# Optimization experiments

Measured on AMD Instinct MI355X. Metric: run time of the kernel, lower is better.

Reference implementation:

```python
import jax, jax.numpy as jnp
import numpy as np

DIM = 512
HEADS = 8
HEAD_DIM = DIM // HEADS
SCALE = HEAD_DIM ** -0.5
LN_EPS = 1e-5


def _layernorm(t, g, b):
    mu = jnp.mean(t, axis=-1, keepdims=True)
    var = jnp.mean(jnp.square(t - mu), axis=-1, keepdims=True)
    return (t - mu) * jax.lax.rsqrt(var + LN_EPS) * g + b


def setup_inputs() -> dict:
    key = jax.random.key(0)
    ks = jax.random.split(key, 8)
    B, C, H, W = 2, DIM, 48, 48
    s = 1.0 / np.sqrt(DIM)
    return {
        "x": jax.random.normal(ks[0], (B, C, H, W), jnp.float32),
        "y": jax.random.normal(ks[1], (B, C, H, W), jnp.float32),
        # linear weights stored [in, out]
        "k_w": jax.random.uniform(ks[2], (DIM, DIM), jnp.float32, -s, s),
        "k_b": jax.random.uniform(ks[3], (DIM,), jnp.float32, -s, s),
        "qv_w": jax.random.uniform(ks[4], (DIM, 2 * DIM), jnp.float32, -s, s),
        "qv_b": jax.random.uniform(ks[5], (2 * DIM,), jnp.float32, -s, s),
        "lnx_g": jnp.ones((DIM,), jnp.float32),
        "lnx_b": jnp.zeros((DIM,), jnp.float32),
        "lny_g": jnp.ones((DIM,), jnp.float32),
        "lny_b": jnp.zeros((DIM,), jnp.float32),
    }


def _split_qv(t, qv_w, qv_b):
    B, N, C = t.shape
    qv = (t @ qv_w + qv_b).reshape(B, N, 2, HEADS, HEAD_DIM)
    qv = jnp.transpose(qv, (2, 0, 3, 1, 4))  # [2, B, h, N, d]
    return qv[0], qv[1]


def _heads(t):
    B, N, C = t.shape
    return jnp.transpose(t.reshape(B, N, HEADS, HEAD_DIM), (0, 2, 1, 3))  # [B,h,N,d]


def reference(x, y, k_w, k_b, qv_w, qv_b, lnx_g, lnx_b, lny_g, lny_b):
    B, C = x.shape[0], x.shape[1]
    xf = _layernorm(jnp.transpose(x.reshape(B, C, -1), (0, 2, 1)), lnx_g, lnx_b)  # [B,N,C]
    yf = _layernorm(jnp.transpose(y.reshape(B, C, -1), (0, 2, 1)), lny_g, lny_b)
    N = xf.shape[1]

    y_q, y_v = _split_qv(yf, qv_w, qv_b)
    x_q, x_v = _split_qv(xf, qv_w, qv_b)
    y_k = _heads(yf @ k_w + k_b)
    x_k = _heads(xf @ k_w + k_b)

    # branch 1: softmax(x_q y_k^T) x_v  -> standard [B,N,C]
    a1 = jax.nn.softmax(jnp.einsum('bhnd,bhmd->bhnm', x_q, y_k) * SCALE, axis=-1)
    xo = jnp.einsum('bhnm,bhmd->bhnd', a1, x_v)
    xo = jnp.transpose(xo, (0, 2, 1, 3)).reshape(B, N, C)

    # branch 2: faithful reproduction of torch quirk (x_k kept a leading 1-dim,
    # so the output [1,B,h,N,d].transpose(1,2).reshape(B,N,C) scrambles layout)
    a2 = jax.nn.softmax(jnp.einsum('bhnd,bhmd->bhnm', y_q, x_k) * SCALE, axis=-1)
    yo = jnp.einsum('bhnm,bhmd->bhnd', a2, y_v)  # [B,h,N,d]
    yo = jnp.transpose(yo[None], (0, 2, 1, 3, 4)).reshape(B, N, C)

    return jnp.concatenate([xo, yo], axis=0)  # [2B, N, C]
```

## Files before the change

### kernel.cpp

```cpp
#include <hip/hip_runtime.h>

#define DIM 512
#define NTOK 2304
#define HEADS 8
#define HD 64
#define LN_EPS 1e-5f
#define BNC 2359296
#define QSC 0.18033688011112042f

typedef __attribute__((ext_vector_type(8))) short short8;
typedef __attribute__((ext_vector_type(4))) short sh4;
typedef __attribute__((ext_vector_type(4))) float f32x4;

__device__ __forceinline__ short f2bf(float f) {
    union { float f; unsigned u; } x; x.f = f;
    unsigned r = (x.u + 0x7fffu + ((x.u >> 16) & 1u)) >> 16;
    return (short)(r & 0xffffu);
}
__device__ __forceinline__ unsigned fbits(float f) {
    union { float f; unsigned u; } x; x.f = f; return x.u;
}
__device__ __forceinline__ void gl2lds(const short* g, short* l) {
    __builtin_amdgcn_global_load_lds(
        (const __attribute__((address_space(1))) unsigned int*)g,
        (__attribute__((address_space(3))) unsigned int*)l, 16, 0, 0);
}

__global__ void k_prep(const float* __restrict__ x, const float* __restrict__ y,
                       float* __restrict__ mu, float* __restrict__ rs,
                       const float* __restrict__ qv_w, const float* __restrict__ k_w,
                       const float* __restrict__ qv_b, const float* __restrict__ k_b,
                       short* __restrict__ Wt, float* __restrict__ bias) {
    __shared__ __align__(16) float tile[64][65];
    __shared__ float pS[4][64], pQ[4][64];
    int bx = blockIdx.x, tid = threadIdx.x;
    if (bx < 144) {
        int nt = bx % 36, sb = bx / 36;
        int nl = tid & 63, part = tid >> 6;
        int n = nt * 64 + nl;
        int s = sb >> 1, b = sb & 1;
        const float* src = (s ? y : x) + (size_t)b * DIM * NTOK + n;
        float sum = 0.f, sq = 0.f;
        for (int c = part * 128; c < part * 128 + 128; c++) {
            float v = src[(size_t)c * NTOK];
            sum += v; sq += v * v;
        }
        pS[part][nl] = sum; pQ[part][nl] = sq;
        __syncthreads();
        if (tid < 64) {
            float ts = pS[0][tid] + pS[1][tid] + pS[2][tid] + pS[3][tid];
            float tq = pQ[0][tid] + pQ[1][tid] + pQ[2][tid] + pQ[3][tid];
            float m = ts * (1.0f / DIM);
            float var = tq * (1.0f / DIM) - m * m;
            mu[sb * NTOK + nt * 64 + tid] = m;
            rs[sb * NTOK + nt * 64 + tid] = rsqrtf(var + LN_EPS);
        }
        return;
    }
    int idx = bx - 144;
    int jt = idx % 24, ct = idx / 24;
    int j0 = jt * 64, c0 = ct * 64;
    if (ct == 0 && tid < 64) {
        int j = j0 + tid;
        bias[j] = (j < 1024) ? qv_b[j] : k_b[j - 1024];
    }
    for (int slot = tid; slot < 1024; slot += 256) {
        int r = slot >> 4, q = slot & 15;
        int c = c0 + r;
        float4 v;
        if (j0 < 1024) v = *(const float4*)(qv_w + (size_t)c * 1024 + j0 + q * 4);
        else           v = *(const float4*)(k_w  + (size_t)c * 512  + (j0 - 1024) + q * 4);
        tile[r][q*4+0] = v.x; tile[r][q*4+1] = v.y;
        tile[r][q*4+2] = v.z; tile[r][q*4+3] = v.w;
    }
    __syncthreads();
    int jr = tid >> 2, cg = tid & 3;
    short8 o0, o1;
    for (int i = 0; i < 8; i++) o0[i] = f2bf(tile[cg*16+i][jr]);
    for (int i = 0; i < 8; i++) o1[i] = f2bf(tile[cg*16+8+i][jr]);
    short* dst = Wt + (size_t)(j0 + jr) * DIM + c0 + cg * 16;
    *(short8*)dst = o0;
    *(short8*)(dst + 8) = o1;
}

__global__ void k_normT(const float* __restrict__ x, const float* __restrict__ y,
                        const float* __restrict__ mu, const float* __restrict__ rs,
                        const float* __restrict__ gx, const float* __restrict__ bx,
                        const float* __restrict__ gy, const float* __restrict__ by,
                        short* __restrict__ T) {
    __shared__ __align__(16) float tile[64][65];
    int nt = blockIdx.x, ct = blockIdx.y, sb = blockIdx.z;
    int s = sb >> 1, b = sb & 1;
    int n0 = nt * 64, c0 = ct * 64;
    const float* src = (s ? y : x) + (size_t)b * DIM * NTOK;
    int tid = threadIdx.x;
    for (int slot = tid; slot < 1024; slot += 256) {
        int r = slot >> 4, q = slot & 15;
        const float* p = src + (size_t)(c0 + r) * NTOK + n0 + q * 4;
        float4 v = *(const float4*)p;
        tile[r][q*4+0] = v.x; tile[r][q*4+1] = v.y;
        tile[r][q*4+2] = v.z; tile[r][q*4+3] = v.w;
    }
    __syncthreads();
    const float* g  = s ? gy : gx;
    const float* be = s ? by : bx;
    int nr = tid >> 2, cg = tid & 3;
    int n = n0 + nr;
    float m = mu[sb * NTOK + n], r_ = rs[sb * NTOK + n];
    short8 o0, o1;
    for (int i = 0; i < 8; i++) {
        int c = c0 + cg * 16 + i;
        o0[i] = f2bf((tile[cg*16+i][nr] - m) * r_ * g[c] + be[c]);
    }
    for (int i = 0; i < 8; i++) {
        int c = c0 + cg * 16 + 8 + i;
        o1[i] = f2bf((tile[cg*16+8+i][nr] - m) * r_ * g[c] + be[c]);
    }
    short* dst = T + ((size_t)sb * NTOK + n) * DIM + c0 + cg * 16;
    *(short8*)dst = o0;
    *(short8*)(dst + 8) = o1;
}

__global__ void __launch_bounds__(256)
k_gemm(const short* __restrict__ T, const short* __restrict__ Wt,
       const float* __restrict__ bias, short* __restrict__ QVK,
       short* __restrict__ VT) {
    __shared__ __align__(16) short smem[2 * 128 * 64];
    short* As = smem;
    short* Bs = smem + 128 * 64;
    int n0 = blockIdx.x * 128, j0 = blockIdx.y * 128, sb = blockIdx.z;
    int tid = threadIdx.x;
    int w = tid >> 6, l = tid & 63;
    int wr = w >> 1, wc = w & 1;
    int lrow = l & 15, quad = l >> 4;
    int r_in = (l >> 3) & 7, cc = l & 7;
    int ch = cc ^ r_in;
    int sw0 = (quad ^ (lrow & 7)) * 8;
    const short* Ab = T + (size_t)sb * NTOK * DIM;
    f32x4 acc[4][4] = {};
    for (int kk = 0; kk < 8; kk++) {
        if (kk) __syncthreads();
        for (int inst = 0; inst < 4; inst++) {
            int R = w * 32 + inst * 8 + r_in;
            gl2lds(Ab + (size_t)(n0 + R) * 512 + kk * 64 + ch * 8,
                   &As[(w * 32 + inst * 8) * 64]);
            gl2lds(Wt + (size_t)(j0 + R) * 512 + kk * 64 + ch * 8,
                   &Bs[(w * 32 + inst * 8) * 64]);
        }
        __syncthreads();
        for (int c2 = 0; c2 < 2; c2++) {
            int off = c2 ? (sw0 ^ 32) : sw0;
            short8 af[4], bf[4];
            for (int i = 0; i < 4; i++)
                af[i] = *(const short8*)&As[(wr*64 + i*16 + lrow) * 64 + off];
            for (int j = 0; j < 4; j++)
                bf[j] = *(const short8*)&Bs[(wc*64 + j*16 + lrow) * 64 + off];
            for (int i = 0; i < 4; i++)
                for (int j = 0; j < 4; j++)
                    acc[i][j] = __builtin_amdgcn_mfma_f32_16x16x32_bf16(af[i], bf[j], acc[i][j], 0, 0, 0);
        }
    }
    if (j0 >= 512 && j0 < 1024) {
        __syncthreads();
        for (int i = 0; i < 4; i++)
            for (int j = 0; j < 4; j++) {
                int jloc = wc * 64 + j * 16 + lrow;
                float bv = bias[j0 + jloc];
                int nloc = wr * 64 + i * 16 + quad * 4;
                int c8 = nloc >> 3, half = (nloc >> 2) & 1;
                sh4 pk;
                for (int reg = 0; reg < 4; reg++) pk[reg] = f2bf(acc[i][j][reg] + bv);
                *(sh4*)&smem[jloc * 128 + ((c8 ^ (jloc & 15)) * 8) + half * 4] = pk;
            }
        __syncthreads();
        for (int slot = tid; slot < 2048; slot += 256) {
            int row = slot >> 4, seg = slot & 15;
            short8 v = *(const short8*)&smem[row * 128 + ((seg ^ (row & 15)) * 8)];
            *(short8*)(VT + ((size_t)sb * 512 + (j0 - 512) + row) * NTOK + n0 + seg * 8) = v;
        }
    } else {
        for (int i = 0; i < 4; i++)
            for (int j = 0; j < 4; j++) {
                int jj = j0 + wc * 64 + j * 16 + lrow;
                float bv = bias[jj];
                float sc = (jj < 512) ? QSC : 1.0f;
                for (int reg = 0; reg < 4; reg++) {
                    int n = n0 + wr * 64 + i * 16 + quad * 4 + reg;
                    QVK[((size_t)sb * NTOK + n) * 1536 + jj] = f2bf((acc[i][j][reg] + bv) * sc);
                }
            }
    }
}

__global__ void __launch_bounds__(256)
k_attn(const short* __restrict__ QVK, const short* __restrict__ VT,
       float* __restrict__ out) {
    __shared__ __align__(16) short Ks[64 * 64];
    __shared__ __align__(16) short Vs[64 * 64];
    __shared__ __align__(16) short Qs[64 * 64];
    int qt = blockIdx.x;
    int yb = blockIdx.y;
    int br = yb >> 4;
    int b  = (yb >> 3) & 1;
    int h  = yb & 7;
    int tid = threadIdx.x;
    int w = tid >> 6, l = tid & 63;
    int lrow = l & 15, quad = l >> 4;
    int r_in = (l >> 3) & 7, cc = l & 7;
    int ch = cc ^ r_in;
    int sw0 = (quad ^ (lrow & 7)) * 8;
    int n0 = qt * 64;
    const short* Qg = QVK + ((size_t)(br * 2 + b) * NTOK) * 1536 + h * 64;
    const short* Kg = QVK + ((size_t)((1 - br) * 2 + b) * NTOK) * 1536 + 1024 + h * 64;
    const short* Vg = VT + ((size_t)(br * 2 + b) * 512 + h * 64) * NTOK;

    for (int inst = 0; inst < 2; inst++) {
        int R = w * 16 + inst * 8 + r_in;
        gl2lds(Qg + (size_t)(n0 + R) * 1536 + ch * 8, &Qs[(w * 16 + inst * 8) * 64]);
    }
    __syncthreads();
    short8 bq0 = *(const short8*)&Qs[(w * 16 + lrow) * 64 + sw0];
    short8 bq1 = *(const short8*)&Qs[(w * 16 + lrow) * 64 + (sw0 ^ 32)];
    short* Pw = &Qs[w * 16 * 64];

    short8 ones;
    for (int i = 0; i < 8; i++) ones[i] = (short)0x3F80;

    f32x4 Oacc[4] = {};
    f32x4 lacc = {};

    for (int mt = 0; mt < 36; mt++) {
        int m0 = mt * 64;
        __syncthreads();
        for (int inst = 0; inst < 2; inst++) {
            int R = w * 16 + inst * 8 + r_in;
            int Rb = (w * 16 + inst * 8) * 64;
            gl2lds(Kg + (size_t)(m0 + R) * 1536 + ch * 8, &Ks[Rb]);
            gl2lds(Vg + (size_t)R * NTOK + m0 + ch * 8, &Vs[Rb]);
        }
        __syncthreads();

        for (int sub = 0; sub < 4; sub++) {
            short8 ak0 = *(const short8*)&Ks[(sub * 16 + lrow) * 64 + sw0];
            short8 ak1 = *(const short8*)&Ks[(sub * 16 + lrow) * 64 + (sw0 ^ 32)];
            f32x4 a = {};
            a = __builtin_amdgcn_mfma_f32_16x16x32_bf16(ak0, bq0, a, 0, 0, 0);
            a = __builtin_amdgcn_mfma_f32_16x16x32_bf16(ak1, bq1, a, 0, 0, 0);
            float p0 = exp2f(a[0]), p1 = exp2f(a[1]);
            float p2 = exp2f(a[2]), p3 = exp2f(a[3]);
            uint2 pk;
            pk.x = __builtin_amdgcn_perm(fbits(p1), fbits(p0), 0x07060302u);
            pk.y = __builtin_amdgcn_perm(fbits(p3), fbits(p2), 0x07060302u);
            *(uint2*)&Pw[lrow * 64 + (((2 * sub + (quad >> 1)) ^ (lrow & 7)) * 8) + (quad & 1) * 4] = pk;
        }

        short8 ap0 = *(const short8*)&Pw[lrow * 64 + sw0];
        short8 ap1 = *(const short8*)&Pw[lrow * 64 + (sw0 ^ 32)];
        lacc = __builtin_amdgcn_mfma_f32_16x16x32_bf16(ones, ap0, lacc, 0, 0, 0);
        lacc = __builtin_amdgcn_mfma_f32_16x16x32_bf16(ones, ap1, lacc, 0, 0, 0);
        for (int ddt = 0; ddt < 4; ddt++) {
            short8 av0 = *(const short8*)&Vs[(ddt * 16 + lrow) * 64 + sw0];
            short8 av1 = *(const short8*)&Vs[(ddt * 16 + lrow) * 64 + (sw0 ^ 32)];
            Oacc[ddt] = __builtin_amdgcn_mfma_f32_16x16x32_bf16(av0, ap0, Oacc[ddt], 0, 0, 0);
            Oacc[ddt] = __builtin_amdgcn_mfma_f32_16x16x32_bf16(av1, ap1, Oacc[ddt], 0, 0, 0);
        }
    }

    float linv = 1.f / lacc[0];
    int n = n0 + w * 16 + lrow;
    for (int ddt = 0; ddt < 4; ddt++) {
        float4 o;
        o.x = Oacc[ddt][0] * linv;
        o.y = Oacc[ddt][1] * linv;
        o.z = Oacc[ddt][2] * linv;
        o.w = Oacc[ddt][3] * linv;
        if (br == 0)
            *(float4*)&out[((size_t)b * NTOK + n) * 512 + h * 64 + ddt * 16 + quad * 4] = o;
        else
            *(float4*)&out[(size_t)BNC + ((size_t)(h * 2 + b) * NTOK + n) * 64 + ddt * 16 + quad * 4] = o;
    }
}

extern "C" void kernel_launch(void* const* d_in, const int* in_sizes, int n_in,
                              void* d_out, int out_size, void* d_ws, size_t ws_size,
                              hipStream_t stream) {
    const float* x     = (const float*)d_in[0];
    const float* y     = (const float*)d_in[1];
    const float* k_w   = (const float*)d_in[2];
    const float* k_b   = (const float*)d_in[3];
    const float* qv_w  = (const float*)d_in[4];
    const float* qv_b  = (const float*)d_in[5];
    const float* lnx_g = (const float*)d_in[6];
    const float* lnx_b = (const float*)d_in[7];
    const float* lny_g = (const float*)d_in[8];
    const float* lny_b = (const float*)d_in[9];
    float* out = (float*)d_out;

    char* ws = (char*)d_ws;
    float* mu   = (float*)ws;
    float* rs   = mu + 9216;
    float* bias = rs + 9216;
    short* T    = (short*)(ws + 79872);
    short* Wt   = T + 4718592;
    short* QVK  = Wt + 786432;
    short* VT   = QVK + 14155776;

    k_prep  <<<336, 256, 0, stream>>>(x, y, mu, rs, qv_w, k_w, qv_b, k_b, Wt, bias);
    k_normT <<<dim3(36, 8, 4), 256, 0, stream>>>(x, y, mu, rs,
                                                 lnx_g, lnx_b, lny_g, lny_b, T);
    k_gemm  <<<dim3(18, 12, 4), 256, 0, stream>>>(T, Wt, bias, QVK, VT);
    k_attn  <<<dim3(36, 32), 256, 0, stream>>>(QVK, VT, out);
}
```

Before: 205.6 us.

## Split attention waves 2x2 over query and key halves, reducing partial outputs via LDS

The attention kernel now assigns each wave 32 query rows and half of each 64-key tile (a 2x2 wave grid), rather than 16 query rows over the full key tile. Each K fragment read from LDS is reused across two query groups and each V fragment across two P groups, which cuts LDS reads per MFMA. Q is loaded straight from global memory into registers, and the P scratch is a padded per-wave buffer. At the end, the two key-half partial sums for O and l are combined through LDS, which adds a reduction step, extra synchronisation and more accumulator registers.

```diff
diff --git a/kernel.cpp b/kernel.cpp
--- a/kernel.cpp
+++ b/kernel.cpp
@@ -197,7 +197,7 @@
        float* __restrict__ out) {
     __shared__ __align__(16) short Ks[64 * 64];
     __shared__ __align__(16) short Vs[64 * 64];
-    __shared__ __align__(16) short Qs[64 * 64];
+    __shared__ __align__(16) short Pbuf[4 * 32 * 40];
     int qt = blockIdx.x;
     int yb = blockIdx.y;
     int br = yb >> 4;
@@ -205,6 +205,7 @@
     int h  = yb & 7;
     int tid = threadIdx.x;
     int w = tid >> 6, l = tid & 63;
+    int wn = w & 1, wm = w >> 1;
     int lrow = l & 15, quad = l >> 4;
     int r_in = (l >> 3) & 7, cc = l & 7;
     int ch = cc ^ r_in;
@@ -213,21 +214,19 @@
     const short* Qg = QVK + ((size_t)(br * 2 + b) * NTOK) * 1536 + h * 64;
     const short* Kg = QVK + ((size_t)((1 - br) * 2 + b) * NTOK) * 1536 + 1024 + h * 64;
     const short* Vg = VT + ((size_t)(br * 2 + b) * 512 + h * 64) * NTOK;
-
-    for (int inst = 0; inst < 2; inst++) {
-        int R = w * 16 + inst * 8 + r_in;
-        gl2lds(Qg + (size_t)(n0 + R) * 1536 + ch * 8, &Qs[(w * 16 + inst * 8) * 64]);
-    }
-    __syncthreads();
-    short8 bq0 = *(const short8*)&Qs[(w * 16 + lrow) * 64 + sw0];
-    short8 bq1 = *(const short8*)&Qs[(w * 16 + lrow) * 64 + (sw0 ^ 32)];
-    short* Pw = &Qs[w * 16 * 64];
+    short* Pw = Pbuf + w * 1280;
+
+    short8 bq[2][2];
+    for (int g = 0; g < 2; g++)
+        for (int h2 = 0; h2 < 2; h2++)
+            bq[g][h2] = *(const short8*)(Qg + (size_t)(n0 + wn * 32 + g * 16 + lrow) * 1536
+                                         + h2 * 32 + quad * 8);
 
     short8 ones;
     for (int i = 0; i < 8; i++) ones[i] = (short)0x3F80;
 
-    f32x4 Oacc[4] = {};
-    f32x4 lacc = {};
+    f32x4 Oacc[4][2] = {};
+    f32x4 lacc[2] = {};
 
     for (int mt = 0; mt < 36; mt++) {
         int m0 = mt * 64;
@@ -240,44 +239,64 @@
         }
         __syncthreads();
 
-        for (int sub = 0; sub < 4; sub++) {
-            short8 ak0 = *(const short8*)&Ks[(sub * 16 + lrow) * 64 + sw0];
-            short8 ak1 = *(const short8*)&Ks[(sub * 16 + lrow) * 64 + (sw0 ^ 32)];
-            f32x4 a = {};
-            a = __builtin_amdgcn_mfma_f32_16x16x32_bf16(ak0, bq0, a, 0, 0, 0);
-            a = __builtin_amdgcn_mfma_f32_16x16x32_bf16(ak1, bq1, a, 0, 0, 0);
-            float p0 = exp2f(a[0]), p1 = exp2f(a[1]);
-            float p2 = exp2f(a[2]), p3 = exp2f(a[3]);
-            uint2 pk;
-            pk.x = __builtin_amdgcn_perm(fbits(p1), fbits(p0), 0x07060302u);
-            pk.y = __builtin_amdgcn_perm(fbits(p3), fbits(p2), 0x07060302u);
-            *(uint2*)&Pw[lrow * 64 + (((2 * sub + (quad >> 1)) ^ (lrow & 7)) * 8) + (quad & 1) * 4] = pk;
-        }
-
-        short8 ap0 = *(const short8*)&Pw[lrow * 64 + sw0];
-        short8 ap1 = *(const short8*)&Pw[lrow * 64 + (sw0 ^ 32)];
-        lacc = __builtin_amdgcn_mfma_f32_16x16x32_bf16(ones, ap0, lacc, 0, 0, 0);
-        lacc = __builtin_amdgcn_mfma_f32_16x16x32_bf16(ones, ap1, lacc, 0, 0, 0);
-        for (int ddt = 0; ddt < 4; ddt++) {
-            short8 av0 = *(const short8*)&Vs[(ddt * 16 + lrow) * 64 + sw0];
-            short8 av1 = *(const short8*)&Vs[(ddt * 16 + lrow) * 64 + (sw0 ^ 32)];
-            Oacc[ddt] = __builtin_amdgcn_mfma_f32_16x16x32_bf16(av0, ap0, Oacc[ddt], 0, 0, 0);
-            Oacc[ddt] = __builtin_amdgcn_mfma_f32_16x16x32_bf16(av1, ap1, Oacc[ddt], 0, 0, 0);
-        }
-    }
-
-    float linv = 1.f / lacc[0];
-    int n = n0 + w * 16 + lrow;
-    for (int ddt = 0; ddt < 4; ddt++) {
-        float4 o;
-        o.x = Oacc[ddt][0] * linv;
-        o.y = Oacc[ddt][1] * linv;
-        o.z = Oacc[ddt][2] * linv;
-        o.w = Oacc[ddt][3] * linv;
-        if (br == 0)
-            *(float4*)&out[((size_t)b * NTOK + n) * 512 + h * 64 + ddt * 16 + quad * 4] = o;
-        else
-            *(float4*)&out[(size_t)BNC + ((size_t)(h * 2 + b) * NTOK + n) * 64 + ddt * 16 + quad * 4] = o;
+        for (int s = 0; s < 2; s++) {
+            int krow = (wm * 32 + s * 16 + lrow) * 64;
+            short8 ak0 = *(const short8*)&Ks[krow + sw0];
+            short8 ak1 = *(const short8*)&Ks[krow + (sw0 ^ 32)];
+            for (int g = 0; g < 2; g++) {
+                f32x4 a = {};
+                a = __builtin_amdgcn_mfma_f32_16x16x32_bf16(ak0, bq[g][0], a, 0, 0, 0);
+                a = __builtin_amdgcn_mfma_f32_16x16x32_bf16(ak1, bq[g][1], a, 0, 0, 0);
+                uint2 pk;
+                pk.x = __builtin_amdgcn_perm(fbits(exp2f(a[1])), fbits(exp2f(a[0])), 0x07060302u);
+                pk.y = __builtin_amdgcn_perm(fbits(exp2f(a[3])), fbits(exp2f(a[2])), 0x07060302u);
+                *(uint2*)&Pw[(g * 16 + lrow) * 40 + s * 16 + quad * 4] = pk;
+            }
+        }
+
+        short8 av[4];
+        for (int dg = 0; dg < 4; dg++)
+            av[dg] = *(const short8*)&Vs[(dg * 16 + lrow) * 64 + (((wm * 4 + quad) ^ (lrow & 7)) * 8)];
+        for (int g = 0; g < 2; g++) {
+            short8 ap = *(const short8*)&Pw[(g * 16 + lrow) * 40 + quad * 8];
+            lacc[g] = __builtin_amdgcn_mfma_f32_16x16x32_bf16(ones, ap, lacc[g], 0, 0, 0);
+            for (int dg = 0; dg < 4; dg++)
+                Oacc[dg][g] = __builtin_amdgcn_mfma_f32_16x16x32_bf16(av[dg], ap, Oacc[dg][g], 0, 0, 0);
+        }
+    }
+
+    __syncthreads();
+    if (wm == 1) {
+        float* dst = (float*)(wn == 0 ? Ks : Vs);
+        for (int dg = 0; dg < 4; dg++)
+            for (int g = 0; g < 2; g++)
+                *(f32x4*)&dst[(dg * 2 + g) * 256 + l * 4] = Oacc[dg][g];
+        ((float*)Pbuf)[wn * 128 + 0 * 64 + l] = lacc[0][0];
+        ((float*)Pbuf)[wn * 128 + 1 * 64 + l] = lacc[1][0];
+    }
+    __syncthreads();
+    if (wm == 0) {
+        float* src = (float*)(wn == 0 ? Ks : Vs);
+        for (int dg = 0; dg < 4; dg++)
+            for (int g = 0; g < 2; g++)
+                Oacc[dg][g] += *(f32x4*)&src[(dg * 2 + g) * 256 + l * 4];
+        float linv[2];
+        for (int g = 0; g < 2; g++)
+            linv[g] = 1.f / (lacc[g][0] + ((float*)Pbuf)[wn * 128 + g * 64 + l]);
+        for (int dg = 0; dg < 4; dg++)
+            for (int g = 0; g < 2; g++) {
+                int n = n0 + wn * 32 + g * 16 + lrow;
+                int d = dg * 16 + quad * 4;
+                float4 o;
+                o.x = Oacc[dg][g][0] * linv[g];
+                o.y = Oacc[dg][g][1] * linv[g];
+                o.z = Oacc[dg][g][2] * linv[g];
+                o.w = Oacc[dg][g][3] * linv[g];
+                if (br == 0)
+                    *(float4*)&out[((size_t)b * NTOK + n) * 512 + h * 64 + d] = o;
+                else
+                    *(float4*)&out[(size_t)BNC + ((size_t)(h * 2 + b) * NTOK + n) * 64 + d] = o;
+            }
     }
 }
 
```

Result: slower. 221.4 us (+7.7%).

## Fuse layernorm stats into normalize-transpose kernel and remap attention blocks per XCD

Applied to the files above, without the earlier changes.

Merges the layernorm statistics pass and the normalize/transpose pass into one kernel. Each tile recomputes its tokens' mean and rstd in shared memory instead of reading them from global workspace, which drops a kernel launch and the mu/rs round trip but reads the input columns eight times redundantly. The attention grid is flattened and remapped so blocks for the same head group are placed on the same XCD, aiming for better L2 reuse of K/V.

```diff
diff --git a/kernel.cpp b/kernel.cpp
--- a/kernel.cpp
+++ b/kernel.cpp
@@ -26,38 +26,68 @@
         (__attribute__((address_space(3))) unsigned int*)l, 16, 0, 0);
 }
 
-__global__ void k_prep(const float* __restrict__ x, const float* __restrict__ y,
-                       float* __restrict__ mu, float* __restrict__ rs,
-                       const float* __restrict__ qv_w, const float* __restrict__ k_w,
-                       const float* __restrict__ qv_b, const float* __restrict__ k_b,
-                       short* __restrict__ Wt, float* __restrict__ bias) {
+__global__ void k_pre(const float* __restrict__ x, const float* __restrict__ y,
+                      const float* __restrict__ qv_w, const float* __restrict__ k_w,
+                      const float* __restrict__ qv_b, const float* __restrict__ k_b,
+                      const float* __restrict__ gx, const float* __restrict__ bx,
+                      const float* __restrict__ gy, const float* __restrict__ by,
+                      short* __restrict__ T, short* __restrict__ Wt,
+                      float* __restrict__ bias) {
     __shared__ __align__(16) float tile[64][65];
     __shared__ float pS[4][64], pQ[4][64];
-    int bx = blockIdx.x, tid = threadIdx.x;
-    if (bx < 144) {
-        int nt = bx % 36, sb = bx / 36;
+    __shared__ float muL[64], rsL[64];
+    int bkid = blockIdx.x, tid = threadIdx.x;
+    if (bkid < 1152) {
+        int nt = bkid % 36, ct = (bkid / 36) % 8, sb = bkid / 288;
+        int s = sb >> 1, b = sb & 1;
+        int n0 = nt * 64, c0 = ct * 64;
+        const float* src = (s ? y : x) + (size_t)b * DIM * NTOK;
         int nl = tid & 63, part = tid >> 6;
-        int n = nt * 64 + nl;
-        int s = sb >> 1, b = sb & 1;
-        const float* src = (s ? y : x) + (size_t)b * DIM * NTOK + n;
-        float sum = 0.f, sq = 0.f;
-        for (int c = part * 128; c < part * 128 + 128; c++) {
-            float v = src[(size_t)c * NTOK];
-            sum += v; sq += v * v;
-        }
-        pS[part][nl] = sum; pQ[part][nl] = sq;
+        {
+            const float* p = src + n0 + nl;
+            float sum = 0.f, sq = 0.f;
+            for (int c = part * 128; c < part * 128 + 128; c++) {
+                float v = p[(size_t)c * NTOK];
+                sum += v; sq += v * v;
+            }
+            pS[part][nl] = sum; pQ[part][nl] = sq;
+        }
         __syncthreads();
         if (tid < 64) {
             float ts = pS[0][tid] + pS[1][tid] + pS[2][tid] + pS[3][tid];
             float tq = pQ[0][tid] + pQ[1][tid] + pQ[2][tid] + pQ[3][tid];
             float m = ts * (1.0f / DIM);
             float var = tq * (1.0f / DIM) - m * m;
-            mu[sb * NTOK + nt * 64 + tid] = m;
-            rs[sb * NTOK + nt * 64 + tid] = rsqrtf(var + LN_EPS);
-        }
+            muL[tid] = m;
+            rsL[tid] = rsqrtf(var + LN_EPS);
+        }
+        for (int slot = tid; slot < 1024; slot += 256) {
+            int r = slot >> 4, q = slot & 15;
+            const float* p = src + (size_t)(c0 + r) * NTOK + n0 + q * 4;
+            float4 v = *(const float4*)p;
+            tile[r][q*4+0] = v.x; tile[r][q*4+1] = v.y;
+            tile[r][q*4+2] = v.z; tile[r][q*4+3] = v.w;
+        }
+        __syncthreads();
+        const float* g  = s ? gy : gx;
+        const float* be = s ? by : bx;
+        int nr = tid >> 2, cg = tid & 3;
+        float m = muL[nr], r_ = rsL[nr];
+        short8 o0, o1;
+        for (int i = 0; i < 8; i++) {
+            int c = c0 + cg * 16 + i;
+            o0[i] = f2bf((tile[cg*16+i][nr] - m) * r_ * g[c] + be[c]);
+        }
+        for (int i = 0; i < 8; i++) {
+            int c = c0 + cg * 16 + 8 + i;
+            o1[i] = f2bf((tile[cg*16+8+i][nr] - m) * r_ * g[c] + be[c]);
+        }
+        short* dst = T + ((size_t)sb * NTOK + n0 + nr) * DIM + c0 + cg * 16;
+        *(short8*)dst = o0;
+        *(short8*)(dst + 8) = o1;
         return;
     }
-    int idx = bx - 144;
+    int idx = bkid - 1152;
     int jt = idx % 24, ct = idx / 24;
     int j0 = jt * 64, c0 = ct * 64;
     if (ct == 0 && tid < 64) {
@@ -79,44 +109,6 @@
     for (int i = 0; i < 8; i++) o0[i] = f2bf(tile[cg*16+i][jr]);
     for (int i = 0; i < 8; i++) o1[i] = f2bf(tile[cg*16+8+i][jr]);
     short* dst = Wt + (size_t)(j0 + jr) * DIM + c0 + cg * 16;
-    *(short8*)dst = o0;
-    *(short8*)(dst + 8) = o1;
-}
-
-__global__ void k_normT(const float* __restrict__ x, const float* __restrict__ y,
-                        const float* __restrict__ mu, const float* __restrict__ rs,
-                        const float* __restrict__ gx, const float* __restrict__ bx,
-                        const float* __restrict__ gy, const float* __restrict__ by,
-                        short* __restrict__ T) {
-    __shared__ __align__(16) float tile[64][65];
-    int nt = blockIdx.x, ct = blockIdx.y, sb = blockIdx.z;
-    int s = sb >> 1, b = sb & 1;
-    int n0 = nt * 64, c0 = ct * 64;
-    const float* src = (s ? y : x) + (size_t)b * DIM * NTOK;
-    int tid = threadIdx.x;
-    for (int slot = tid; slot < 1024; slot += 256) {
-        int r = slot >> 4, q = slot & 15;
-        const float* p = src + (size_t)(c0 + r) * NTOK + n0 + q * 4;
-        float4 v = *(const float4*)p;
-        tile[r][q*4+0] = v.x; tile[r][q*4+1] = v.y;
-        tile[r][q*4+2] = v.z; tile[r][q*4+3] = v.w;
-    }
-    __syncthreads();
-    const float* g  = s ? gy : gx;
-    const float* be = s ? by : bx;
-    int nr = tid >> 2, cg = tid & 3;
-    int n = n0 + nr;
-    float m = mu[sb * NTOK + n], r_ = rs[sb * NTOK + n];
-    short8 o0, o1;
-    for (int i = 0; i < 8; i++) {
-        int c = c0 + cg * 16 + i;
-        o0[i] = f2bf((tile[cg*16+i][nr] - m) * r_ * g[c] + be[c]);
-    }
-    for (int i = 0; i < 8; i++) {
-        int c = c0 + cg * 16 + 8 + i;
-        o1[i] = f2bf((tile[cg*16+8+i][nr] - m) * r_ * g[c] + be[c]);
-    }
-    short* dst = T + ((size_t)sb * NTOK + n) * DIM + c0 + cg * 16;
     *(short8*)dst = o0;
     *(short8*)(dst + 8) = o1;
 }
@@ -198,8 +190,10 @@
     __shared__ __align__(16) short Ks[64 * 64];
     __shared__ __align__(16) short Vs[64 * 64];
     __shared__ __align__(16) short Qs[64 * 64];
-    int qt = blockIdx.x;
-    int yb = blockIdx.y;
+    int id = blockIdx.x;
+    int xcd = id & 7, rem = id >> 3;
+    int qt = rem % 36, yhi = rem / 36;
+    int yb = yhi * 8 + xcd;
     int br = yb >> 4;
     int b  = (yb >> 3) & 1;
     int h  = yb & 7;
@@ -297,17 +291,14 @@
     float* out = (float*)d_out;
 
     char* ws = (char*)d_ws;
-    float* mu   = (float*)ws;
-    float* rs   = mu + 9216;
-    float* bias = rs + 9216;
-    short* T    = (short*)(ws + 79872);
+    float* bias = (float*)ws;
+    short* T    = (short*)(ws + 6144);
     short* Wt   = T + 4718592;
     short* QVK  = Wt + 786432;
     short* VT   = QVK + 14155776;
 
-    k_prep  <<<336, 256, 0, stream>>>(x, y, mu, rs, qv_w, k_w, qv_b, k_b, Wt, bias);
-    k_normT <<<dim3(36, 8, 4), 256, 0, stream>>>(x, y, mu, rs,
-                                                 lnx_g, lnx_b, lny_g, lny_b, T);
-    k_gemm  <<<dim3(18, 12, 4), 256, 0, stream>>>(T, Wt, bias, QVK, VT);
-    k_attn  <<<dim3(36, 32), 256, 0, stream>>>(QVK, VT, out);
-}
+    k_pre  <<<1344, 256, 0, stream>>>(x, y, qv_w, k_w, qv_b, k_b,
+                                      lnx_g, lnx_b, lny_g, lny_b, T, Wt, bias);
+    k_gemm <<<dim3(18, 12, 4), 256, 0, stream>>>(T, Wt, bias, QVK, VT);
+    k_attn <<<1152, 256, 0, stream>>>(QVK, VT, out);
+}
```

Result: no change. 202.6 us (-1.4%).
